# Kernel tuning notes

Hardware: AMD Instinct MI355X
Metric: run time of the kernel (lower is better)

Reference implementation:

```python
import jax, jax.numpy as jnp
from jax import lax
import numpy as np

MAX_FLARES = 6
NMS_KERNEL = 9
CONF_THRESHOLD = 0.3


def setup_inputs() -> dict:
    key = jax.random.key(0)
    heatmap = jax.random.uniform(key, (64, 1, 640, 640), dtype=jnp.float32)
    return {"heatmap": heatmap}


def reference(heatmap):
    # heatmap: [B, 1, H, W]
    B, _, H, W = heatmap.shape
    K = MAX_FLARES
    hm = heatmap[:, 0]  # [B, H, W]

    # NMS via max-pool: kernel NMS_KERNEL, stride 1, SAME padding (pad = k//2)
    hm_max = lax.reduce_window(
        hm, -jnp.inf, lax.max,
        window_dimensions=(1, NMS_KERNEL, NMS_KERNEL),
        window_strides=(1, 1, 1),
        padding="SAME",
    )
    peaks = (hm == hm_max) & (hm > CONF_THRESHOLD)  # [B, H, W] bool
    scores = jnp.where(peaks, hm, jnp.float32(0.0))  # suppressed -> 0

    # Batched top-K over flattened spatial dims (replaces per-batch Python loop)
    flat = scores.reshape(B, H * W)
    top_scores, top_idx = lax.top_k(flat, K)  # [B, K] each, sorted desc

    # A slot is valid iff its score is a true peak (> threshold). Since all
    # non-peak entries were zeroed, this exactly reproduces the original's
    # min(K, n_peaks) truncation + `break` on sub-threshold scores.
    valid = top_scores > CONF_THRESHOLD  # [B, K]

    xs_grid = jnp.linspace(0.0, 1.0, W, dtype=hm.dtype)
    ys_grid = jnp.linspace(0.0, 1.0, H, dtype=hm.dtype)
    x_idx = top_idx % W
    y_idx = top_idx // W

    pos_x = jnp.where(valid, xs_grid[x_idx], jnp.float32(-1.0))
    pos_y = jnp.where(valid, ys_grid[y_idx], jnp.float32(-1.0))
    pred_positions = jnp.stack([pos_x, pos_y], axis=-1)  # [B, K, 2]
    pred_conf = jnp.where(valid, top_scores, jnp.float32(0.0))  # [B, K]
    return pred_positions, pred_conf
```

## Files before the change

### kernel.cpp

```cpp
#include <hip/hip_runtime.h>
#include <float.h>
#include <stdint.h>

#define HH 640
#define WW 640
#define KTOP 6
#define CONF 0.3f
#define NTHR 256
#define ROWS_W 16
#define XBANDS 3
#define XOUT 248
#define YWAVES (HH / ROWS_W)
#define TASKS_PER_B (XBANDS * YWAVES)
#define MENT (TASKS_PER_B * KTOP)
#define CAP 128

__device__ __forceinline__ float4 f4max(float4 a, float4 b) {
    return make_float4(fmaxf(a.x, b.x), fmaxf(a.y, b.y), fmaxf(a.z, b.z), fmaxf(a.w, b.w));
}

__device__ __forceinline__ float dpp_up(float v) {
    return __int_as_float(__builtin_amdgcn_update_dpp(
        (int)0xFF800000, __float_as_int(v), 0x138, 0xF, 0xF, false));
}
__device__ __forceinline__ float dpp_dn(float v) {
    return __int_as_float(__builtin_amdgcn_update_dpp(
        (int)0xFF800000, __float_as_int(v), 0x130, 0xF, 0xF, false));
}

__global__ __launch_bounds__(NTHR, 3) void peaks_kernel(const float* __restrict__ hm,
                                                        float* __restrict__ bscore,
                                                        int* __restrict__ bidx) {
    __shared__ float c_score[4][CAP];
    __shared__ int   c_idx[4][CAP];
    __shared__ int   c_cnt[4];

    const int t    = threadIdx.x;
    const int lane = t & 63;
    const int w    = t >> 6;
    const int task = blockIdx.x * 4 + w;
    const int b    = task / TASKS_PER_B;
    const int rem  = task - b * TASKS_PER_B;
    const int yw   = rem / XBANDS;
    const int xb   = rem - yw * XBANDS;
    const int ybase = yw * ROWS_W;
    const int x_raw = xb * XOUT - 4 + 4 * lane;
    const int xc    = min(max(x_raw, 0), WW - 4);
    const bool xok  = (x_raw >= 0) && (x_raw <= WW - 4);
    const bool vlane = (lane >= 1) && (lane <= 62) && xok;
    const float* colp = hm + (size_t)b * (HH * WW) + xc;
    const float4 NEG = make_float4(-FLT_MAX, -FLT_MAX, -FLT_MAX, -FLT_MAX);

    if (lane == 0) c_cnt[w] = 0;

    float4 r0, r1, r2, r3, r4, r5, r6, r7, r8, r9, r10, r11,
           r12, r13, r14, r15, r16, r17, r18, r19, r20, r21, r22, r23;
    #define LDA(i, dst) { int gy = ybase - 4 + (i); \
        gy = gy < 0 ? 0 : (gy > HH - 1 ? HH - 1 : gy); \
        const float* ap = colp + (size_t)gy * WW; \
        asm volatile("global_load_dwordx4 %0, %1, off" : "=&v"(dst) : "v"(ap)); }
    LDA(0,  r0)  LDA(1,  r1)  LDA(2,  r2)  LDA(3,  r3)
    LDA(4,  r4)  LDA(5,  r5)  LDA(6,  r6)  LDA(7,  r7)
    LDA(8,  r8)  LDA(9,  r9)  LDA(10, r10) LDA(11, r11)
    LDA(12, r12) LDA(13, r13) LDA(14, r14) LDA(15, r15)
    LDA(16, r16) LDA(17, r17) LDA(18, r18) LDA(19, r19)
    LDA(20, r20) LDA(21, r21) LDA(22, r22) LDA(23, r23)

    #define PROCROW(m, c, gy_) { \
        const float a_ = fmaxf(m.y, m.z); \
        const float w0 = dpp_up(m.x), ha = dpp_up(a_), w2 = dpp_up(m.z), w3 = dpp_up(m.w); \
        const float w8 = dpp_dn(m.x), w9 = dpp_dn(m.y), hb = dpp_dn(a_), wB = dpp_dn(m.w); \
        const float mc = fmaxf(fmaxf(m.x, a_), m.w); \
        const float hc = fmaxf(fmaxf(w3, mc), w8); \
        const float h0 = fmaxf(hc, fmaxf(w0, ha)); \
        const float h1 = fmaxf(hc, fmaxf(ha, w9)); \
        const float h2 = fmaxf(hc, fmaxf(w2, hb)); \
        const float h3 = fmaxf(hc, fmaxf(hb, wB)); \
        if (vlane) { \
            const int base = (gy_) * WW + x_raw; \
            if (c.x > CONF && c.x >= h0) { int p_ = atomicAdd(&c_cnt[w], 1); if (p_ < CAP) { c_score[w][p_] = c.x; c_idx[w][p_] = base;     } } \
            if (c.y > CONF && c.y >= h1) { int p_ = atomicAdd(&c_cnt[w], 1); if (p_ < CAP) { c_score[w][p_] = c.y; c_idx[w][p_] = base + 1; } } \
            if (c.z > CONF && c.z >= h2) { int p_ = atomicAdd(&c_cnt[w], 1); if (p_ < CAP) { c_score[w][p_] = c.z; c_idx[w][p_] = base + 2; } } \
            if (c.w > CONF && c.w >= h3) { int p_ = atomicAdd(&c_cnt[w], 1); if (p_ < CAP) { c_score[w][p_] = c.w; c_idx[w][p_] = base + 3; } } \
        } \
    }

    #define VROW(Sx, c, gy_) { \
        float4 m = f4max(Sx, pref); \
        if (!xok) m = NEG; \
        PROCROW(m, c, gy_) \
    }

    asm volatile("s_waitcnt vmcnt(8)" ::: "memory");
    __builtin_amdgcn_sched_barrier(0);
    {
        float4 S7 = r7;
        float4 S6 = f4max(r6, S7), S5 = f4max(r5, S6), S4 = f4max(r4, S5);
        float4 S3 = f4max(r3, S4), S2 = f4max(r2, S3), S1 = f4max(r1, S2), S0 = f4max(r0, S1);
        float4 pref = r8;
        VROW(S0, r4,  ybase + 0)  pref = f4max(pref, r9);
        VROW(S1, r5,  ybase + 1)  pref = f4max(pref, r10);
        VROW(S2, r6,  ybase + 2)  pref = f4max(pref, r11);
        VROW(S3, r7,  ybase + 3)  pref = f4max(pref, r12);
        VROW(S4, r8,  ybase + 4)  pref = f4max(pref, r13);
        VROW(S5, r9,  ybase + 5)  pref = f4max(pref, r14);
        VROW(S6, r10, ybase + 6)  pref = f4max(pref, r15);
        VROW(S7, r11, ybase + 7)
    }

    asm volatile("s_waitcnt vmcnt(0)" ::: "memory");
    __builtin_amdgcn_sched_barrier(0);
    {
        float4 S7 = r15;
        float4 S6 = f4max(r14, S7), S5 = f4max(r13, S6), S4 = f4max(r12, S5);
        float4 S3 = f4max(r11, S4), S2 = f4max(r10, S3), S1 = f4max(r9, S2), S0 = f4max(r8, S1);
        float4 pref = r16;
        VROW(S0, r12, ybase + 8)   pref = f4max(pref, r17);
        VROW(S1, r13, ybase + 9)   pref = f4max(pref, r18);
        VROW(S2, r14, ybase + 10)  pref = f4max(pref, r19);
        VROW(S3, r15, ybase + 11)  pref = f4max(pref, r20);
        VROW(S4, r16, ybase + 12)  pref = f4max(pref, r21);
        VROW(S5, r17, ybase + 13)  pref = f4max(pref, r22);
        VROW(S6, r18, ybase + 14)  pref = f4max(pref, r23);
        VROW(S7, r19, ybase + 15)
    }

    {
        const int cnt = min(c_cnt[w], CAP);
        float cs0 = (lane      < cnt) ? c_score[w][lane]      : -2.0f;
        int   ci0 = (lane      < cnt) ? c_idx[w][lane]        : 0x7fffffff;
        float cs1 = (lane + 64 < cnt) ? c_score[w][lane + 64] : -2.0f;
        int   ci1 = (lane + 64 < cnt) ? c_idx[w][lane + 64]   : 0x7fffffff;
        const int outbase = task * KTOP;
        #pragma unroll
        for (int k = 0; k < KTOP; ++k) {
            float bs; int bi;
            if (cs0 > cs1 || (cs0 == cs1 && ci0 < ci1)) { bs = cs0; bi = ci0; }
            else                                        { bs = cs1; bi = ci1; }
            #pragma unroll
            for (int off = 32; off >= 1; off >>= 1) {
                const float os = __shfl_xor(bs, off);
                const int   oi = __shfl_xor(bi, off);
                if (os > bs || (os == bs && oi < bi)) { bs = os; bi = oi; }
            }
            if (lane == 0) { bscore[outbase + k] = bs; bidx[outbase + k] = bi; }
            if (ci0 == bi) cs0 = -3.0f;
            if (ci1 == bi) cs1 = -3.0f;
        }
    }
}

__global__ __launch_bounds__(64) void topk_kernel(const float* __restrict__ bscore,
                                                  const int* __restrict__ bidx,
                                                  float* __restrict__ out,
                                                  int B) {
    const int t = threadIdx.x;
    const int b = blockIdx.x;

    float s[12]; int id[12];
    #pragma unroll
    for (int j = 0; j < 12; ++j) {
        const int e = t + 64 * j;
        const bool ok = e < MENT;
        s[j]  = ok ? bscore[b * MENT + e] : -9.0f;
        id[j] = ok ? bidx[b * MENT + e]   : 0x7fffffff;
    }

    float my_s = -9.0f; int my_i = 0x7fffffff;
    #pragma unroll
    for (int k = 0; k < KTOP; ++k) {
        float bs = s[0]; int bi = id[0];
        #pragma unroll
        for (int j = 1; j < 12; ++j)
            if (s[j] > bs || (s[j] == bs && id[j] < bi)) { bs = s[j]; bi = id[j]; }
        #pragma unroll
        for (int off = 32; off >= 1; off >>= 1) {
            const float os = __shfl_xor(bs, off);
            const int   oi = __shfl_xor(bi, off);
            if (os > bs || (os == bs && oi < bi)) { bs = os; bi = oi; }
        }
        if (t == k) { my_s = bs; my_i = bi; }
        #pragma unroll
        for (int j = 0; j < 12; ++j) if (id[j] == bi) s[j] = -9.0f;
    }

    if (t < KTOP) {
        const bool valid = (my_s > CONF) && (my_i >= 0) && (my_i < HH * WW);
        const int idv = valid ? my_i : 0;
        const int xi = idv % WW;
        const int yi = idv / WW;
        const float px = valid ? xi * (1.0f / (WW - 1)) : -1.0f;
        const float py = valid ? yi * (1.0f / (HH - 1)) : -1.0f;
        out[(size_t)b * KTOP * 2 + t * 2 + 0] = px;
        out[(size_t)b * KTOP * 2 + t * 2 + 1] = py;
        out[(size_t)B * KTOP * 2 + (size_t)b * KTOP + t] = valid ? my_s : 0.0f;
    }
}

extern "C" void kernel_launch(void* const* d_in, const int* in_sizes, int n_in,
                              void* d_out, int out_size, void* d_ws, size_t ws_size,
                              hipStream_t stream) {
    const float* hm = (const float*)d_in[0];
    float* out = (float*)d_out;
    const int B = in_sizes[0] / (HH * WW);

    float* bscore = (float*)d_ws;
    int*   bidx   = (int*)((char*)d_ws + sizeof(float) * (size_t)B * MENT);

    const int nblocks = (B * TASKS_PER_B) / 4;
    peaks_kernel<<<nblocks, NTHR, 0, stream>>>(hm, bscore, bidx);
    topk_kernel<<<B, 64, 0, stream>>>(bscore, bidx, out, B);
}
```

Before: 163.7 us.

## Share vertical halo rows between stacked waves through LDS

Each block now covers 64 consecutive rows with its four waves stacked vertically. Interior halo rows are exchanged through shared memory instead of each wave reloading 8 extra rows, and only the top and bottom waves fetch the block-edge halos. This cuts global loads from 24 to about 16 rows per wave. In exchange it adds LDS traffic, a block-wide barrier, and a full vmcnt(0) wait that removes the earlier two-phase load overlap, and occupancy is lowered to 2 blocks.

```diff
diff --git a/kernel.cpp b/kernel.cpp
--- a/kernel.cpp
+++ b/kernel.cpp
@@ -8,10 +8,11 @@
 #define CONF 0.3f
 #define NTHR 256
 #define ROWS_W 16
+#define ROWS_B 64
 #define XBANDS 3
 #define XOUT 248
-#define YWAVES (HH / ROWS_W)
-#define TASKS_PER_B (XBANDS * YWAVES)
+#define YBLK (HH / ROWS_B)
+#define TASKS_PER_B (XBANDS * YBLK * 4)
 #define MENT (TASKS_PER_B * KTOP)
 #define CAP 128
 
@@ -28,9 +29,11 @@
         (int)0xFF800000, __float_as_int(v), 0x130, 0xF, 0xF, false));
 }
 
-__global__ __launch_bounds__(NTHR, 3) void peaks_kernel(const float* __restrict__ hm,
+__global__ __launch_bounds__(NTHR, 2) void peaks_kernel(const float* __restrict__ hm,
                                                         float* __restrict__ bscore,
                                                         int* __restrict__ bidx) {
+    __shared__ float lds_below[4][4][256];
+    __shared__ float lds_above[4][4][256];
     __shared__ float c_score[4][CAP];
     __shared__ int   c_idx[4][CAP];
     __shared__ int   c_cnt[4];
@@ -38,13 +41,10 @@
     const int t    = threadIdx.x;
     const int lane = t & 63;
     const int w    = t >> 6;
-    const int task = blockIdx.x * 4 + w;
-    const int b    = task / TASKS_PER_B;
-    const int rem  = task - b * TASKS_PER_B;
-    const int yw   = rem / XBANDS;
-    const int xb   = rem - yw * XBANDS;
-    const int ybase = yw * ROWS_W;
-    const int x_raw = xb * XOUT - 4 + 4 * lane;
+    const int b    = blockIdx.z;
+    const int yb0  = blockIdx.y * ROWS_B;
+    const int yw0  = yb0 + w * ROWS_W;
+    const int x_raw = blockIdx.x * XOUT - 4 + 4 * lane;
     const int xc    = min(max(x_raw, 0), WW - 4);
     const bool xok  = (x_raw >= 0) && (x_raw <= WW - 4);
     const bool vlane = (lane >= 1) && (lane <= 62) && xok;
@@ -53,18 +53,56 @@
 
     if (lane == 0) c_cnt[w] = 0;
 
-    float4 r0, r1, r2, r3, r4, r5, r6, r7, r8, r9, r10, r11,
-           r12, r13, r14, r15, r16, r17, r18, r19, r20, r21, r22, r23;
-    #define LDA(i, dst) { int gy = ybase - 4 + (i); \
+    float4 r0, r1, r2, r3, r4, r5, r6, r7, r8, r9, r10, r11, r12, r13, r14, r15;
+    float4 e0, e1, e2, e3;
+    #define LDA(dst, yy) { int gy = (yy); \
         gy = gy < 0 ? 0 : (gy > HH - 1 ? HH - 1 : gy); \
         const float* ap = colp + (size_t)gy * WW; \
         asm volatile("global_load_dwordx4 %0, %1, off" : "=&v"(dst) : "v"(ap)); }
-    LDA(0,  r0)  LDA(1,  r1)  LDA(2,  r2)  LDA(3,  r3)
-    LDA(4,  r4)  LDA(5,  r5)  LDA(6,  r6)  LDA(7,  r7)
-    LDA(8,  r8)  LDA(9,  r9)  LDA(10, r10) LDA(11, r11)
-    LDA(12, r12) LDA(13, r13) LDA(14, r14) LDA(15, r15)
-    LDA(16, r16) LDA(17, r17) LDA(18, r18) LDA(19, r19)
-    LDA(20, r20) LDA(21, r21) LDA(22, r22) LDA(23, r23)
+    LDA(r0,  yw0 + 0)  LDA(r1,  yw0 + 1)  LDA(r2,  yw0 + 2)  LDA(r3,  yw0 + 3)
+    LDA(r4,  yw0 + 4)  LDA(r5,  yw0 + 5)  LDA(r6,  yw0 + 6)  LDA(r7,  yw0 + 7)
+    LDA(r8,  yw0 + 8)  LDA(r9,  yw0 + 9)  LDA(r10, yw0 + 10) LDA(r11, yw0 + 11)
+    LDA(r12, yw0 + 12) LDA(r13, yw0 + 13) LDA(r14, yw0 + 14) LDA(r15, yw0 + 15)
+    if (w == 0) { LDA(e0, yw0 - 4)  LDA(e1, yw0 - 3)  LDA(e2, yw0 - 2)  LDA(e3, yw0 - 1) }
+    if (w == 3) { LDA(e0, yw0 + 16) LDA(e1, yw0 + 17) LDA(e2, yw0 + 18) LDA(e3, yw0 + 19) }
+
+    asm volatile("s_waitcnt vmcnt(0)" ::: "memory");
+
+    const int lc = 4 * lane;
+    if (w > 0) {
+        *reinterpret_cast<float4*>(&lds_above[w - 1][0][lc]) = r0;
+        *reinterpret_cast<float4*>(&lds_above[w - 1][1][lc]) = r1;
+        *reinterpret_cast<float4*>(&lds_above[w - 1][2][lc]) = r2;
+        *reinterpret_cast<float4*>(&lds_above[w - 1][3][lc]) = r3;
+    }
+    if (w < 3) {
+        *reinterpret_cast<float4*>(&lds_below[w + 1][0][lc]) = r12;
+        *reinterpret_cast<float4*>(&lds_below[w + 1][1][lc]) = r13;
+        *reinterpret_cast<float4*>(&lds_below[w + 1][2][lc]) = r14;
+        *reinterpret_cast<float4*>(&lds_below[w + 1][3][lc]) = r15;
+    }
+    if (w == 0) {
+        *reinterpret_cast<float4*>(&lds_below[0][0][lc]) = e0;
+        *reinterpret_cast<float4*>(&lds_below[0][1][lc]) = e1;
+        *reinterpret_cast<float4*>(&lds_below[0][2][lc]) = e2;
+        *reinterpret_cast<float4*>(&lds_below[0][3][lc]) = e3;
+    }
+    if (w == 3) {
+        *reinterpret_cast<float4*>(&lds_above[3][0][lc]) = e0;
+        *reinterpret_cast<float4*>(&lds_above[3][1][lc]) = e1;
+        *reinterpret_cast<float4*>(&lds_above[3][2][lc]) = e2;
+        *reinterpret_cast<float4*>(&lds_above[3][3][lc]) = e3;
+    }
+    __syncthreads();
+
+    const float4 b0 = *reinterpret_cast<const float4*>(&lds_below[w][0][lc]);
+    const float4 b1 = *reinterpret_cast<const float4*>(&lds_below[w][1][lc]);
+    const float4 b2 = *reinterpret_cast<const float4*>(&lds_below[w][2][lc]);
+    const float4 b3 = *reinterpret_cast<const float4*>(&lds_below[w][3][lc]);
+    const float4 a0 = *reinterpret_cast<const float4*>(&lds_above[w][0][lc]);
+    const float4 a1 = *reinterpret_cast<const float4*>(&lds_above[w][1][lc]);
+    const float4 a2 = *reinterpret_cast<const float4*>(&lds_above[w][2][lc]);
+    const float4 a3 = *reinterpret_cast<const float4*>(&lds_above[w][3][lc]);
 
     #define PROCROW(m, c, gy_) { \
         const float a_ = fmaxf(m.y, m.z); \
@@ -84,45 +122,39 @@
             if (c.w > CONF && c.w >= h3) { int p_ = atomicAdd(&c_cnt[w], 1); if (p_ < CAP) { c_score[w][p_] = c.w; c_idx[w][p_] = base + 3; } } \
         } \
     }
-
     #define VROW(Sx, c, gy_) { \
         float4 m = f4max(Sx, pref); \
         if (!xok) m = NEG; \
         PROCROW(m, c, gy_) \
     }
 
-    asm volatile("s_waitcnt vmcnt(8)" ::: "memory");
-    __builtin_amdgcn_sched_barrier(0);
     {
-        float4 S7 = r7;
-        float4 S6 = f4max(r6, S7), S5 = f4max(r5, S6), S4 = f4max(r4, S5);
-        float4 S3 = f4max(r3, S4), S2 = f4max(r2, S3), S1 = f4max(r1, S2), S0 = f4max(r0, S1);
-        float4 pref = r8;
-        VROW(S0, r4,  ybase + 0)  pref = f4max(pref, r9);
-        VROW(S1, r5,  ybase + 1)  pref = f4max(pref, r10);
-        VROW(S2, r6,  ybase + 2)  pref = f4max(pref, r11);
-        VROW(S3, r7,  ybase + 3)  pref = f4max(pref, r12);
-        VROW(S4, r8,  ybase + 4)  pref = f4max(pref, r13);
-        VROW(S5, r9,  ybase + 5)  pref = f4max(pref, r14);
-        VROW(S6, r10, ybase + 6)  pref = f4max(pref, r15);
-        VROW(S7, r11, ybase + 7)
-    }
-
-    asm volatile("s_waitcnt vmcnt(0)" ::: "memory");
-    __builtin_amdgcn_sched_barrier(0);
+        float4 S7 = r3;
+        float4 S6 = f4max(r2, S7), S5 = f4max(r1, S6), S4 = f4max(r0, S5);
+        float4 S3 = f4max(b3, S4), S2 = f4max(b2, S3), S1 = f4max(b1, S2), S0 = f4max(b0, S1);
+        float4 pref = r4;
+        VROW(S0, r0, yw0 + 0)  pref = f4max(pref, r5);
+        VROW(S1, r1, yw0 + 1)  pref = f4max(pref, r6);
+        VROW(S2, r2, yw0 + 2)  pref = f4max(pref, r7);
+        VROW(S3, r3, yw0 + 3)  pref = f4max(pref, r8);
+        VROW(S4, r4, yw0 + 4)  pref = f4max(pref, r9);
+        VROW(S5, r5, yw0 + 5)  pref = f4max(pref, r10);
+        VROW(S6, r6, yw0 + 6)  pref = f4max(pref, r11);
+        VROW(S7, r7, yw0 + 7)
+    }
     {
-        float4 S7 = r15;
-        float4 S6 = f4max(r14, S7), S5 = f4max(r13, S6), S4 = f4max(r12, S5);
-        float4 S3 = f4max(r11, S4), S2 = f4max(r10, S3), S1 = f4max(r9, S2), S0 = f4max(r8, S1);
-        float4 pref = r16;
-        VROW(S0, r12, ybase + 8)   pref = f4max(pref, r17);
-        VROW(S1, r13, ybase + 9)   pref = f4max(pref, r18);
-        VROW(S2, r14, ybase + 10)  pref = f4max(pref, r19);
-        VROW(S3, r15, ybase + 11)  pref = f4max(pref, r20);
-        VROW(S4, r16, ybase + 12)  pref = f4max(pref, r21);
-        VROW(S5, r17, ybase + 13)  pref = f4max(pref, r22);
-        VROW(S6, r18, ybase + 14)  pref = f4max(pref, r23);
-        VROW(S7, r19, ybase + 15)
+        float4 S7 = r11;
+        float4 S6 = f4max(r10, S7), S5 = f4max(r9, S6), S4 = f4max(r8, S5);
+        float4 S3 = f4max(r7, S4), S2 = f4max(r6, S3), S1 = f4max(r5, S2), S0 = f4max(r4, S1);
+        float4 pref = r12;
+        VROW(S0, r8,  yw0 + 8)   pref = f4max(pref, r13);
+        VROW(S1, r9,  yw0 + 9)   pref = f4max(pref, r14);
+        VROW(S2, r10, yw0 + 10)  pref = f4max(pref, r15);
+        VROW(S3, r11, yw0 + 11)  pref = f4max(pref, a0);
+        VROW(S4, r12, yw0 + 12)  pref = f4max(pref, a1);
+        VROW(S5, r13, yw0 + 13)  pref = f4max(pref, a2);
+        VROW(S6, r14, yw0 + 14)  pref = f4max(pref, a3);
+        VROW(S7, r15, yw0 + 15)
     }
 
     {
@@ -131,7 +163,8 @@
         int   ci0 = (lane      < cnt) ? c_idx[w][lane]        : 0x7fffffff;
         float cs1 = (lane + 64 < cnt) ? c_score[w][lane + 64] : -2.0f;
         int   ci1 = (lane + 64 < cnt) ? c_idx[w][lane + 64]   : 0x7fffffff;
-        const int outbase = task * KTOP;
+        const int outbase = ((b * YBLK + blockIdx.y) * 4 + w) * XBANDS * KTOP
+                            + blockIdx.x * KTOP;
         #pragma unroll
         for (int k = 0; k < KTOP; ++k) {
             float bs; int bi;
@@ -207,7 +240,7 @@
     float* bscore = (float*)d_ws;
     int*   bidx   = (int*)((char*)d_ws + sizeof(float) * (size_t)B * MENT);
 
-    const int nblocks = (B * TASKS_PER_B) / 4;
-    peaks_kernel<<<nblocks, NTHR, 0, stream>>>(hm, bscore, bidx);
+    dim3 grid1(XBANDS, YBLK, B);
+    peaks_kernel<<<grid1, NTHR, 0, stream>>>(hm, bscore, bidx);
     topk_kernel<<<B, 64, 0, stream>>>(bscore, bidx, out, B);
 }
```

Result: slower. 167.6 us (+2.4%).
